# Kernel optimization log

Hardware: AMD Instinct MI355X
Metric: run time of the kernel (lower is better)

The kernel has to match this reference:

```python
import jax, jax.numpy as jnp
import numpy as np

B, C, W, H, HEADS = 8, 512, 32, 32, 8
DH = C // HEADS  # 64
N = W * H        # 1024


def setup_inputs() -> dict:
    key = jax.random.key(0)
    ks = jax.random.split(key, 10)
    s = 1.0 / np.sqrt(C)
    return {
        "x": jax.random.normal(ks[0], (B, C, W, H), jnp.float32),
        "d": jax.random.normal(ks[1], (B, C, W, H), jnp.float32),
        "Wq": jax.random.normal(ks[2], (C, C), jnp.float32) * s,
        "bq": jnp.zeros((C,), jnp.float32),
        "Wk": jax.random.normal(ks[3], (C, C), jnp.float32) * s,
        "bk": jnp.zeros((C,), jnp.float32),
        "Wv": jax.random.normal(ks[4], (C, C), jnp.float32) * s,
        "bv": jnp.zeros((C,), jnp.float32),
        "rel_h": jax.random.normal(ks[5], (1, HEADS, DH, 1, H), jnp.float32),
        "rel_w": jax.random.normal(ks[6], (1, HEADS, DH, W, 1), jnp.float32),
    }


def reference(x, d, Wq, bq, Wk, bk, Wv, bv, rel_h, rel_w):
    b, c, w, h = x.shape
    heads = rel_h.shape[1]
    dh = c // heads
    n = w * h

    def proj(t, Wt, bt):
        # 1x1 conv == per-pixel channel matmul; reshape to [B, heads, dh, N]
        y = jnp.einsum('bchw,oc->bohw', t, Wt) + bt[None, :, None, None]
        return y.reshape(b, heads, dh, n)

    q = proj(x, Wq, bq)
    k = proj(d, Wk, bk)
    v = proj(d, Wv, bv)

    # content-content: q^T k -> [B, h, N, N]
    cc = jnp.einsum('bhdn,bhdm->bhnm', q, k)
    # content-position: (rel_h + rel_w) broadcast -> [1, h, dh, N], then pos^T @ q
    pos = (rel_h + rel_w).reshape(heads, dh, n)
    cp = jnp.einsum('hdm,bhdn->bhmn', pos, q)

    attn = jax.nn.softmax(cc + cp, axis=-1)  # [B, h, N, N]
    # out = v @ attn^T : out[b,h,d,i] = sum_j v[b,h,d,j] * attn[b,h,i,j]
    out = jnp.einsum('bhdj,bhij->bhdi', v, attn)
    return out.reshape(b, c, w, h)
```

## Files before the change

### kernel.cpp

```cpp
#include <hip/hip_runtime.h>

typedef unsigned short u16;
typedef _Float16 f16x8 __attribute__((ext_vector_type(8)));
typedef __fp16 hf16x2 __attribute__((ext_vector_type(2)));
typedef float f32x4 __attribute__((ext_vector_type(4)));
typedef float f32x16 __attribute__((ext_vector_type(16)));
typedef unsigned uint2v __attribute__((ext_vector_type(2)));

#define NB 8
#define NC 512
#define NHD 8
#define DH 64
#define NN 1024
#define LOG2E 1.4426950408889634f

__device__ __forceinline__ u16 f2h(float f) {
    union { _Float16 h; u16 u; } v; v.h = (_Float16)f;
    return v.u;
}

__global__ __launch_bounds__(256) void k_prep(
    const float* __restrict__ x, const float* __restrict__ d,
    const float* __restrict__ Wq, const float* __restrict__ Wk, const float* __restrict__ Wv,
    const float* __restrict__ relh, const float* __restrict__ relw,
    u16* __restrict__ xt, u16* __restrict__ dt,
    u16* __restrict__ wq, u16* __restrict__ wk, u16* __restrict__ wv,
    u16* __restrict__ ps) {
    __shared__ float tile[64][65];
    int id = blockIdx.x, t = threadIdx.x;
    if (id < 2048) {
        int nb = (id & 15) * 64;
        int cb = ((id >> 4) & 7) * 64;
        int z = id >> 7;
        int b = z & 7;
        const float* src = (z >> 3) ? d : x;
        u16* ot = (z >> 3) ? dt : xt;
        {
            int crow = t >> 2, n0 = (t & 3) * 16;
            const float* g = src + ((size_t)(b * NC + cb + crow)) * NN + nb + n0;
#pragma unroll
            for (int k = 0; k < 16; k += 4) {
                float4 v = *(const float4*)(g + k);
                tile[crow][n0 + k + 0] = v.x;
                tile[crow][n0 + k + 1] = v.y;
                tile[crow][n0 + k + 2] = v.z;
                tile[crow][n0 + k + 3] = v.w;
            }
        }
        __syncthreads();
        {
            int nrow = t >> 2, c0 = (t & 3) * 16;
            union { u16 s[16]; uint4 v[2]; } uh;
#pragma unroll
            for (int k = 0; k < 16; ++k) uh.s[k] = f2h(tile[c0 + k][nrow]);
            size_t oidx = ((size_t)(b * NN + nb + nrow)) * NC + cb + c0;
            *(uint4*)(ot + oidx)     = uh.v[0];
            *(uint4*)(ot + oidx + 8) = uh.v[1];
        }
    } else if (id < 5120) {
        int j = id - 2048;
        int m = j >> 10;
        int i = (j & 1023) * 256 + t;
        const float* src = (m == 0) ? Wq : (m == 1) ? Wk : Wv;
        u16* dst = (m == 0) ? wq : (m == 1) ? wk : wv;
        dst[i] = f2h(src[i]);
    } else {
        int idx = (id - 5120) * 256 + t;
        int dd = idx & 63;
        int i  = (idx >> 6) & 1023;
        int h  = idx >> 16;
        float f = relh[(h * 64 + dd) * 32 + (i & 31)] + relw[(h * 64 + dd) * 32 + (i >> 5)];
        ps[(h * 1024 + i) * 64 + dd] = f2h(f);
    }
}

__global__ __launch_bounds__(256) void k_proj(
    const u16* __restrict__ xt, const u16* __restrict__ dt,
    const u16* __restrict__ wq, const u16* __restrict__ wk, const u16* __restrict__ wv,
    const float* __restrict__ bq, const float* __restrict__ bk, const float* __restrict__ bv,
    u16* __restrict__ qt_o, u16* __restrict__ kt_o, u16* __restrict__ v_o) {
    __shared__ u16 Asm[128 * 32];
    __shared__ u16 Bsm[128 * 32];

    int p = blockIdx.z % 3;
    int b = blockIdx.z / 3;
    const u16 *Ap, *Bp;
    const float* bias;
    u16* Oq;
    if (p == 0)      { Ap = wq; Bp = xt; bias = bq; Oq = qt_o; }
    else if (p == 1) { Ap = wk; Bp = dt; bias = bk; Oq = kt_o; }
    else             { Ap = wv; Bp = dt; bias = bv; Oq = v_o; }
    Bp += (size_t)b * NN * NC;
    float oscale = (p == 0) ? LOG2E : 1.0f;

    int obase = blockIdx.x * 128;
    int nbase = blockIdx.y * 128;
    int t = threadIdx.x, wave = t >> 6, quad = (t & 63) >> 4, l15 = t & 15;
    int wr = (wave >> 1) * 64, wc = (wave & 1) * 64;

    f32x4 acc[4][4];
#pragma unroll
    for (int fo = 0; fo < 4; ++fo)
#pragma unroll
        for (int fn = 0; fn < 4; ++fn)
#pragma unroll
            for (int r = 0; r < 4; ++r) acc[fo][fn][r] = 0.f;

    for (int kk = 0; kk < NC; kk += 32) {
        __syncthreads();
#pragma unroll
        for (int u = 0; u < 2; ++u) {
            int c = u * 256 + t;
            int row = c >> 2, part = c & 3;
            __builtin_amdgcn_global_load_lds(
                (const __attribute__((address_space(1))) void*)(Ap + (size_t)(obase + row) * NC + kk + part * 8),
                (__attribute__((address_space(3))) void*)(Asm + (size_t)(u * 256 + wave * 64) * 8), 16, 0, 0);
            __builtin_amdgcn_global_load_lds(
                (const __attribute__((address_space(1))) void*)(Bp + (size_t)(nbase + row) * NC + kk + part * 8),
                (__attribute__((address_space(3))) void*)(Bsm + (size_t)(u * 256 + wave * 64) * 8), 16, 0, 0);
        }
        __syncthreads();

        f16x8 af[4], bfr[4];
#pragma unroll
        for (int fo = 0; fo < 4; ++fo) af[fo] = *(const f16x8*)&Asm[(wr + fo * 16 + l15) * 32 + quad * 8];
#pragma unroll
        for (int fn = 0; fn < 4; ++fn) bfr[fn] = *(const f16x8*)&Bsm[(wc + fn * 16 + l15) * 32 + quad * 8];
#pragma unroll
        for (int fo = 0; fo < 4; ++fo)
#pragma unroll
            for (int fn = 0; fn < 4; ++fn)
                acc[fo][fn] = __builtin_amdgcn_mfma_f32_16x16x32_f16(af[fo], bfr[fn], acc[fo][fn], 0, 0, 0);
    }

#pragma unroll
    for (int fo = 0; fo < 4; ++fo) {
#pragma unroll
        for (int fn = 0; fn < 4; ++fn) {
            int o0 = obase + wr + fo * 16 + quad * 4;
            int n = nbase + wc + fn * 16 + l15;
            if (p < 2) {
                union { u16 s[4]; uint2 v2; } uh;
#pragma unroll
                for (int r = 0; r < 4; ++r) uh.s[r] = f2h((acc[fo][fn][r] + bias[o0 + r]) * oscale);
                int head = o0 >> 6, dd0 = o0 & 63;
                size_t idx = (((size_t)(b * NHD + head) * NN) + n) * DH + dd0;
                *(uint2*)&Oq[idx] = uh.v2;
            } else {
#pragma unroll
                for (int r = 0; r < 4; ++r) {
                    int o = o0 + r;
                    int head = o >> 6, dd = o & 63;
                    Oq[((size_t)(b * NHD + head) * DH + dd) * NN + n] = f2h(acc[fo][fn][r] + bias[o]);
                }
            }
        }
    }
}

__global__ __launch_bounds__(256, 2) void k_attn(
    const u16* __restrict__ qt, const u16* __restrict__ kt,
    const u16* __restrict__ v_, const u16* __restrict__ pos,
    float* __restrict__ out) {
    __shared__ u16 Bs[128 * 132];
    __shared__ u16 Vt[64 * 132];

    int n = blockIdx.x;
    int g = n & 63;
    int ib = n >> 6;
    int head = g & 7, b = g >> 3;

    int t = threadIdx.x, ws = t >> 6, lane = t & 63, h = lane >> 5, l31 = lane & 31;
    size_t bh = (size_t)(b * NHD + head);
    const u16* qb = qt + bh * NN * DH;
    const u16* kb = kt + bh * NN * DH;
    const u16* vb = v_ + bh * DH * NN;
    const u16* pb = pos + (size_t)head * NN * DH;
    int i0 = ib * 128;
    int iglob = i0 + ws * 32 + l31;

    f16x8 qf[8];
#pragma unroll
    for (int ks = 0; ks < 4; ++ks) qf[ks] = *(const f16x8*)&qb[(size_t)iglob * DH + ks * 16 + h * 8];
#pragma unroll
    for (int ks = 4; ks < 8; ++ks) qf[ks] = *(const f16x8*)&pb[(size_t)iglob * DH + (ks - 4) * 16 + h * 8];

    f32x16 oacc[2];
#pragma unroll
    for (int df = 0; df < 2; ++df)
#pragma unroll
        for (int r = 0; r < 16; ++r) oacc[df][r] = 0.f;
    float m_ = -__builtin_inff(), l_ = 0.f;

    for (int jc = 0; jc < NN; jc += 128) {
        __syncthreads();
#pragma unroll
        for (int u = 0; u < 8; ++u) {
            int c = u * 256 + t;
            int row = c >> 4, gg = c & 15;
            const u16* src = (gg < 8) ? &kb[(size_t)(jc + row) * DH + gg * 8]
                                      : &qb[(size_t)(jc + row) * DH + (gg - 8) * 8];
            *(uint4*)&Bs[row * 132 + gg * 8] = *(const uint4*)src;
        }
#pragma unroll
        for (int u = 0; u < 4; ++u) {
            int c = u * 256 + t;
            int row = c >> 4, gg = c & 15;
            *(uint4*)&Vt[row * 132 + gg * 8] = *(const uint4*)&vb[(size_t)row * NN + jc + gg * 8];
        }
        __syncthreads();

        f32x16 sacc[4];
#pragma unroll
        for (int jf = 0; jf < 4; ++jf)
#pragma unroll
            for (int r = 0; r < 16; ++r) sacc[jf][r] = 0.f;
        __builtin_amdgcn_s_setprio(1);
#pragma unroll
        for (int jf = 0; jf < 4; ++jf)
#pragma unroll
            for (int ks = 0; ks < 8; ++ks) {
                f16x8 af = *(const f16x8*)&Bs[(jf * 32 + l31) * 132 + ks * 16 + h * 8];
                sacc[jf] = __builtin_amdgcn_mfma_f32_32x32x16_f16(af, qf[ks], sacc[jf], 0, 0, 0);
            }
        __builtin_amdgcn_s_setprio(0);

        float mloc = -__builtin_inff();
#pragma unroll
        for (int jf = 0; jf < 4; ++jf)
#pragma unroll
            for (int r = 0; r < 16; ++r) mloc = fmaxf(mloc, sacc[jf][r]);
        mloc = fmaxf(mloc, __shfl_xor(mloc, 32));
        if (__any(mloc - m_ > 8.f)) {
            float mnew = fmaxf(m_, mloc);
            float alpha = __builtin_amdgcn_exp2f(m_ - mnew);
            m_ = mnew;
#pragma unroll
            for (int df = 0; df < 2; ++df)
#pragma unroll
                for (int r = 0; r < 16; ++r) oacc[df][r] *= alpha;
            l_ *= alpha;
        }
        float lsum = 0.f;
#pragma unroll
        for (int jf = 0; jf < 4; ++jf)
#pragma unroll
            for (int r = 0; r < 16; ++r) {
                float pv = __builtin_amdgcn_exp2f(sacc[jf][r] - m_);
                sacc[jf][r] = pv;
                lsum += pv;
            }
        lsum += __shfl_xor(lsum, 32);
        l_ += lsum;

        __builtin_amdgcn_s_setprio(1);
#pragma unroll
        for (int jw = 0; jw < 8; ++jw) {
            int jf = jw >> 1, r0 = (jw & 1) * 8;
            union { hf16x2 v; unsigned u; } a0, a1, b0, b1;
            a0.v = __builtin_amdgcn_cvt_pkrtz(sacc[jf][r0 + 0], sacc[jf][r0 + 1]);
            a1.v = __builtin_amdgcn_cvt_pkrtz(sacc[jf][r0 + 2], sacc[jf][r0 + 3]);
            b0.v = __builtin_amdgcn_cvt_pkrtz(sacc[jf][r0 + 4], sacc[jf][r0 + 5]);
            b1.v = __builtin_amdgcn_cvt_pkrtz(sacc[jf][r0 + 6], sacc[jf][r0 + 7]);
            uint2v s0 = __builtin_amdgcn_permlane32_swap(a0.u, b0.u, false, false);
            uint2v s1 = __builtin_amdgcn_permlane32_swap(a1.u, b1.u, false, false);
            union { unsigned w[4]; f16x8 f; } pf;
            pf.w[0] = s0.x;
            pf.w[1] = s1.x;
            pf.w[2] = s0.y;
            pf.w[3] = s1.y;
#pragma unroll
            for (int df = 0; df < 2; ++df) {
                f16x8 vf = *(const f16x8*)&Vt[(df * 32 + l31) * 132 + jw * 16 + h * 8];
                oacc[df] = __builtin_amdgcn_mfma_f32_32x32x16_f16(vf, pf.f, oacc[df], 0, 0, 0);
            }
        }
        __builtin_amdgcn_s_setprio(0);
    }

    float li = 1.0f / l_;
#pragma unroll
    for (int df = 0; df < 2; ++df)
#pragma unroll
        for (int r = 0; r < 16; ++r) {
            int dd = df * 32 + (r & 3) + 8 * (r >> 2) + 4 * h;
            out[((size_t)(b * NC) + head * DH + dd) * NN + i0 + ws * 32 + l31] = oacc[df][r] * li;
        }
}

#define SXT  (8u * 1024u * 512u * 2u)
#define SW   (512u * 512u * 2u)
#define SQT  SXT
#define SPOS (8u * 1024u * 64u * 2u)

#define OFF_XT   (0u)
#define OFF_DT   (OFF_XT + SXT)
#define OFF_WQ   (OFF_DT + SXT)
#define OFF_WK   (OFF_WQ + SW)
#define OFF_WV   (OFF_WK + SW)
#define OFF_QT   (OFF_WV + SW)
#define OFF_KT   (OFF_QT + SQT)
#define OFF_V    (OFF_KT + SQT)
#define OFF_POS  (OFF_V + SQT)

extern "C" void kernel_launch(void* const* d_in, const int* in_sizes, int n_in,
                              void* d_out, int out_size, void* d_ws, size_t ws_size,
                              hipStream_t stream) {
    const float* x   = (const float*)d_in[0];
    const float* d   = (const float*)d_in[1];
    const float* Wq  = (const float*)d_in[2];
    const float* bq  = (const float*)d_in[3];
    const float* Wk  = (const float*)d_in[4];
    const float* bk  = (const float*)d_in[5];
    const float* Wv  = (const float*)d_in[6];
    const float* bv  = (const float*)d_in[7];
    const float* rh  = (const float*)d_in[8];
    const float* rw  = (const float*)d_in[9];

    char* ws = (char*)d_ws;
    u16* xt = (u16*)(ws + OFF_XT);
    u16* dt = (u16*)(ws + OFF_DT);
    u16* wq = (u16*)(ws + OFF_WQ);
    u16* wk = (u16*)(ws + OFF_WK);
    u16* wv = (u16*)(ws + OFF_WV);
    u16* qt = (u16*)(ws + OFF_QT);
    u16* kt = (u16*)(ws + OFF_KT);
    u16* v_ = (u16*)(ws + OFF_V);
    u16* ps = (u16*)(ws + OFF_POS);

    k_prep<<<7168, 256, 0, stream>>>(x, d, Wq, Wk, Wv, rh, rw, xt, dt, wq, wk, wv, ps);
    k_proj<<<dim3(4, 8, 24), 256, 0, stream>>>(xt, dt, wq, wk, wv, bq, bk, bv, qt, kt, v_);
    k_attn<<<512, 256, 0, stream>>>(qt, kt, v_, ps, (float*)d_out);
}
```

Baseline: 165.2 us.

## Prefetch next K/Q/V tile into registers, vectorize weight convert, split softmax reductions

The attention kernel now loads the next 128-column chunk of K, Q and V from global memory into registers while the current chunk's MFMAs and softmax run, and only writes it to LDS at the start of the next iteration. This is meant to hide global load latency behind compute. The weight fp32-to-fp16 conversion in the prep kernel now uses float4 loads and 4-wide stores, with the grid shrunk to match. The row max and sum reductions are split into four independent chains to shorten dependency latency. The 12 extra uint4 registers per thread raise register pressure and may lower occupancy.

Result: slower. 217.8 us (+31.8%).

```diff
diff --git a/kernel.cpp b/kernel.cpp
--- a/kernel.cpp
+++ b/kernel.cpp
@@ -57,15 +57,19 @@
             *(uint4*)(ot + oidx)     = uh.v[0];
             *(uint4*)(ot + oidx + 8) = uh.v[1];
         }
-    } else if (id < 5120) {
+    } else if (id < 2816) {
         int j = id - 2048;
-        int m = j >> 10;
-        int i = (j & 1023) * 256 + t;
+        int m = j >> 8;
+        int blk = j & 255;
         const float* src = (m == 0) ? Wq : (m == 1) ? Wk : Wv;
         u16* dst = (m == 0) ? wq : (m == 1) ? wk : wv;
-        dst[i] = f2h(src[i]);
+        int i = (blk * 256 + t) * 4;
+        float4 v = *(const float4*)(src + i);
+        union { u16 s[4]; uint2 u2; } r;
+        r.s[0] = f2h(v.x); r.s[1] = f2h(v.y); r.s[2] = f2h(v.z); r.s[3] = f2h(v.w);
+        *(uint2*)(dst + i) = r.u2;
     } else {
-        int idx = (id - 5120) * 256 + t;
+        int idx = (id - 2816) * 256 + t;
         int dd = idx & 63;
         int i  = (idx >> 6) & 1023;
         int h  = idx >> 16;
@@ -192,23 +196,48 @@
         for (int r = 0; r < 16; ++r) oacc[df][r] = 0.f;
     float m_ = -__builtin_inff(), l_ = 0.f;
 
+    uint4 sA[12];
+#pragma unroll
+    for (int u = 0; u < 8; ++u) {
+        int c = u * 256 + t; int row = c >> 4, gg = c & 15;
+        const u16* src = (gg < 8) ? &kb[(size_t)row * DH + gg * 8]
+                                  : &qb[(size_t)row * DH + (gg - 8) * 8];
+        sA[u] = *(const uint4*)src;
+    }
+#pragma unroll
+    for (int u = 0; u < 4; ++u) {
+        int c = u * 256 + t; int row = c >> 4, gg = c & 15;
+        sA[8 + u] = *(const uint4*)&vb[(size_t)row * NN + gg * 8];
+    }
+
     for (int jc = 0; jc < NN; jc += 128) {
         __syncthreads();
 #pragma unroll
         for (int u = 0; u < 8; ++u) {
             int c = u * 256 + t;
-            int row = c >> 4, gg = c & 15;
-            const u16* src = (gg < 8) ? &kb[(size_t)(jc + row) * DH + gg * 8]
-                                      : &qb[(size_t)(jc + row) * DH + (gg - 8) * 8];
-            *(uint4*)&Bs[row * 132 + gg * 8] = *(const uint4*)src;
+            *(uint4*)&Bs[(c >> 4) * 132 + (c & 15) * 8] = sA[u];
         }
 #pragma unroll
         for (int u = 0; u < 4; ++u) {
             int c = u * 256 + t;
-            int row = c >> 4, gg = c & 15;
-            *(uint4*)&Vt[row * 132 + gg * 8] = *(const uint4*)&vb[(size_t)row * NN + jc + gg * 8];
-        }
-        __syncthreads();
+            *(uint4*)&Vt[(c >> 4) * 132 + (c & 15) * 8] = sA[8 + u];
+        }
+        __syncthreads();
+        if (jc + 128 < NN) {
+            int jn = jc + 128;
+#pragma unroll
+            for (int u = 0; u < 8; ++u) {
+                int c = u * 256 + t; int row = c >> 4, gg = c & 15;
+                const u16* src = (gg < 8) ? &kb[(size_t)(jn + row) * DH + gg * 8]
+                                          : &qb[(size_t)(jn + row) * DH + (gg - 8) * 8];
+                sA[u] = *(const uint4*)src;
+            }
+#pragma unroll
+            for (int u = 0; u < 4; ++u) {
+                int c = u * 256 + t; int row = c >> 4, gg = c & 15;
+                sA[8 + u] = *(const uint4*)&vb[(size_t)row * NN + jn + gg * 8];
+            }
+        }
 
         f32x16 sacc[4];
 #pragma unroll
@@ -225,11 +254,19 @@
             }
         __builtin_amdgcn_s_setprio(0);
 
-        float mloc = -__builtin_inff();
-#pragma unroll
-        for (int jf = 0; jf < 4; ++jf)
-#pragma unroll
-            for (int r = 0; r < 16; ++r) mloc = fmaxf(mloc, sacc[jf][r]);
+        float mj[4];
+#pragma unroll
+        for (int jf = 0; jf < 4; ++jf) {
+            float a = fmaxf(fmaxf(sacc[jf][0], sacc[jf][1]), sacc[jf][2]);
+            a = fmaxf(fmaxf(a, sacc[jf][3]), sacc[jf][4]);
+            a = fmaxf(fmaxf(a, sacc[jf][5]), sacc[jf][6]);
+            a = fmaxf(fmaxf(a, sacc[jf][7]), sacc[jf][8]);
+            a = fmaxf(fmaxf(a, sacc[jf][9]), sacc[jf][10]);
+            a = fmaxf(fmaxf(a, sacc[jf][11]), sacc[jf][12]);
+            a = fmaxf(fmaxf(a, sacc[jf][13]), sacc[jf][14]);
+            mj[jf] = fmaxf(a, sacc[jf][15]);
+        }
+        float mloc = fmaxf(fmaxf(mj[0], mj[1]), fmaxf(mj[2], mj[3]));
         mloc = fmaxf(mloc, __shfl_xor(mloc, 32));
         if (__any(mloc - m_ > 8.f)) {
             float mnew = fmaxf(m_, mloc);
@@ -241,15 +278,19 @@
                 for (int r = 0; r < 16; ++r) oacc[df][r] *= alpha;
             l_ *= alpha;
         }
-        float lsum = 0.f;
-#pragma unroll
-        for (int jf = 0; jf < 4; ++jf)
+        float ls[4];
+#pragma unroll
+        for (int jf = 0; jf < 4; ++jf) {
+            float s = 0.f;
 #pragma unroll
             for (int r = 0; r < 16; ++r) {
                 float pv = __builtin_amdgcn_exp2f(sacc[jf][r] - m_);
                 sacc[jf][r] = pv;
-                lsum += pv;
-            }
+                s += pv;
+            }
+            ls[jf] = s;
+        }
+        float lsum = (ls[0] + ls[1]) + (ls[2] + ls[3]);
         lsum += __shfl_xor(lsum, 32);
         l_ += lsum;
 
@@ -328,7 +369,7 @@
     u16* v_ = (u16*)(ws + OFF_V);
     u16* ps = (u16*)(ws + OFF_POS);
 
-    k_prep<<<7168, 256, 0, stream>>>(x, d, Wq, Wk, Wv, rh, rw, xt, dt, wq, wk, wv, ps);
+    k_prep<<<4864, 256, 0, stream>>>(x, d, Wq, Wk, Wv, rh, rw, xt, dt, wq, wk, wv, ps);
     k_proj<<<dim3(4, 8, 24), 256, 0, stream>>>(xt, dt, wq, wk, wv, bq, bk, bv, qt, kt, v_);
     k_attn<<<512, 256, 0, stream>>>(qt, kt, v_, ps, (float*)d_out);
 }
```
